# Optimization experiments

Hardware: AMD Instinct MI355X
Metric: run time of the kernel (lower is better)

Reference implementation:

```python
import jax, jax.numpy as jnp
import numpy as np

N_CONST = 188
P = 16
HIDDEN = 128
DE = 5
DO = 6
N_TARGETS = 5
BATCH = 32


def _edge_indices(n):
    # receiver/sender pairs in the same order as itertools.product, skipping diagonal
    r, s = np.meshgrid(np.arange(n), np.arange(n), indexing='ij')
    mask = r != s
    return jnp.asarray(r[mask]), jnp.asarray(s[mask])  # each [n*(n-1)]


def _linear_params(key, fan_in, fan_out):
    kw, kb = jax.random.split(key)
    w = jax.random.normal(kw, (fan_in, fan_out), jnp.float32) / np.sqrt(fan_in)
    b = jax.random.normal(kb, (fan_out,), jnp.float32) * 0.01
    return w, b


def setup_inputs() -> dict:
    key = jax.random.key(0)
    ks = jax.random.split(key, 10)
    inp = {"x": jax.random.normal(ks[0], (BATCH, N_CONST, P), jnp.float32)}
    h2 = HIDDEN // 2
    dims = [
        ("fr1", 2 * P, HIDDEN), ("fr2", HIDDEN, h2), ("fr3", h2, DE),
        ("fo1", P + DE, HIDDEN), ("fo2", HIDDEN, h2), ("fo3", h2, DO),
        ("fc1", DO * N_CONST, HIDDEN), ("fc2", HIDDEN, h2), ("fc3", h2, N_TARGETS),
    ]
    for i, (name, fi, fo) in enumerate(dims):
        w, b = _linear_params(ks[i + 1], fi, fo)
        inp[name + "_w"] = w
        inp[name + "_b"] = b
    return inp


def reference(x, fr1_w, fr1_b, fr2_w, fr2_b, fr3_w, fr3_b,
              fo1_w, fo1_b, fo2_w, fo2_b, fo3_w, fo3_b,
              fc1_w, fc1_b, fc2_w, fc2_b, fc3_w, fc3_b):
    B, n, p = x.shape
    recv, send = _edge_indices(n)  # [Nr]
    # gather receiver/sender node features (replaces one-hot matmuls with Rr, Rs)
    e_in = jnp.concatenate([x[:, recv], x[:, send]], axis=-1)  # [B, Nr, 2P]
    h = jax.nn.relu(e_in @ fr1_w + fr1_b)
    h = jax.nn.relu(h @ fr2_w + fr2_b)
    E = jax.nn.relu(h @ fr3_w + fr3_b)  # [B, Nr, De]
    # scatter-add edge effects back to receiver nodes (replaces E @ Rr^T)
    Ebar = jnp.zeros((B, n, E.shape[-1]), x.dtype).at[:, recv].add(E)  # [B, N, De]
    c = jnp.concatenate([x, Ebar], axis=-1)  # [B, N, P+De]
    h = jax.nn.relu(c @ fo1_w + fo1_b)
    h = jax.nn.relu(h @ fo2_w + fo2_b)
    O = jax.nn.relu(h @ fo3_w + fo3_b)  # [B, N, Do]
    h = jax.nn.relu(O.reshape(B, -1) @ fc1_w + fc1_b)
    h = jax.nn.relu(h @ fc2_w + fc2_b)
    return h @ fc3_w + fc3_b  # [B, n_targets]
```

## Files before the change

kernel.cpp:

```cpp
#include <hip/hip_runtime.h>

#define BB   32
#define NN   188
#define PP   16
#define HID  128
#define HH2  64
#define DE   5
#define DO   6
#define NT   5
#define ROWS_O (BB*NN)
#define RT   32
#define KO   (PP+DE)

typedef __attribute__((ext_vector_type(8))) short short8;
typedef __attribute__((ext_vector_type(4))) float float4_;

__device__ __forceinline__ short f2bf(float v) {
    union { float f; unsigned u; } a; a.f = v;
    unsigned r = a.u + 0x7fff + ((a.u >> 16) & 1);
    return (short)(r >> 16);
}
__device__ __forceinline__ unsigned r2u(float v) {
    v = v > 0.f ? v : 0.f;
    return __float_as_uint(v) + 0x8000u;
}
__device__ __forceinline__ unsigned pack_hi16(unsigned hi, unsigned lo) {
    return __builtin_amdgcn_perm(hi, lo, 0x07060302);
}

#define XB_OFF    0
#define XB_ELTS   (BB*NN*24)
#define W1T_OFF   (XB_OFF + XB_ELTS)
#define W1T_ELTS  (HID*40)
#define W2S_OFF   (W1T_OFF + W1T_ELTS)
#define W2S_ELTS  (16*64*8)
#define W3S_OFF   (W2S_OFF + W2S_ELTS)
#define W3S_ELTS  (2*64*8)
#define SHORT_TOTAL (W3S_OFF + W3S_ELTS)
#define WFRAG_UINT4 ((W2S_ELTS + W3S_ELTS) * 2 / 16)

__device__ __forceinline__ int pinv(int pk) {
    return ((pk >> 5) * 2 + (pk & 1)) * 16 + ((pk & 31) >> 1);
}

__global__ void prep_kernel(const float* __restrict__ x,
                            const float* __restrict__ w1,
                            const float* __restrict__ w2,
                            const float* __restrict__ w3,
                            short* __restrict__ ws)
{
    const int i = blockIdx.x * blockDim.x + threadIdx.x;
    const int stride = gridDim.x * blockDim.x;
    for (int idx = i; idx < BB*NN*PP; idx += stride) {
        int row = idx >> 4, k = idx & 15;
        ws[XB_OFF + row*24 + k] = f2bf(x[idx]);
    }
    for (int idx = i; idx < 32*HID; idx += stride) {
        int k = idx >> 7, n = idx & 127;
        ws[W1T_OFF + n*40 + k] = f2bf(w1[idx]);
    }
    for (int idx = i; idx < W2S_ELTS; idx += stride) {
        int f = idx >> 9;
        int l = (idx >> 3) & 63;
        int e = idx & 7;
        int t = f >> 2, s = f & 3;
        int q = l >> 4, n16 = l & 15;
        int pk = s*32 + q*8 + e;
        int k = pinv(pk);
        int n = t*16 + n16;
        ws[W2S_OFF + idx] = f2bf(w2[k*HH2 + n]);
    }
    for (int idx = i; idx < W3S_ELTS; idx += stride) {
        int s = idx >> 9;
        int l = (idx >> 3) & 63;
        int e = idx & 7;
        int q = l >> 4, n16 = l & 15;
        int pk = s*32 + q*8 + e;
        int k = pinv(pk);
        ws[W3S_OFF + idx] = (n16 < DE) ? f2bf(w3[k*DE + n16]) : (short)0;
    }
}

__global__ __launch_bounds__(256)
void edge_mfma_kernel(const short* __restrict__ ws_s,
                      const float* __restrict__ b1,
                      const float* __restrict__ b2,
                      const float* __restrict__ b3,
                      float* __restrict__ ebar)
{
    const short* xb  = ws_s + XB_OFF;
    const short* w1t = ws_s + W1T_OFF;

    __shared__ __align__(16) unsigned wsmem[4608];
    __shared__ __align__(16) unsigned h1d[4][16*68];
    __shared__ __align__(16) unsigned h2d[4][16*36];
    __shared__ float red[4][8];

    const int bi   = blockIdx.x;
    const int b    = bi / NN;
    const int recv = bi - b*NN;
    const int tid  = threadIdx.x;
    const int wave = tid >> 6;
    const int lane = tid & 63;
    const int n16  = lane & 15;
    const int q    = lane >> 4;

    {
        const uint4* src = (const uint4*)(ws_s + W2S_OFF);
        uint4* dst = (uint4*)wsmem;
        #pragma unroll
        for (int i = 0; i < 5; ++i) {
            int idx = tid + i*256;
            if (idx < WFRAG_UINT4) dst[idx] = src[idx];
        }
    }

    short8 B1[8];
    #pragma unroll
    for (int t = 0; t < 8; ++t)
        B1[t] = *(const short8*)(w1t + (t*16 + n16)*40 + q*8);

    float bias1[8];
    #pragma unroll
    for (int t = 0; t < 8; ++t) bias1[t] = b1[t*16 + n16];
    float bias2[4];
    #pragma unroll
    for (int t = 0; t < 4; ++t) bias2[t] = b2[t*16 + n16];
    const float bias3 = (n16 < DE) ? b3[n16] : 0.f;

    __syncthreads();

    const short* w2l = (const short*)wsmem;
    const short* w3l = (const short*)(wsmem + 4096);
    short8 B3[2];
    #pragma unroll
    for (int s = 0; s < 2; ++s)
        B3[s] = *(const short8*)(w3l + s*512 + lane*8);

    const short* xrow = xb + b*(NN*24);
    unsigned* h1w = &h1d[wave][0];
    unsigned* h2w = &h2d[wave][0];
    const short* h1r = (const short*)h1w;
    const short* h2r = (const short*)h2w;

    float acc[4] = {0.f, 0.f, 0.f, 0.f};

    #pragma unroll
    for (int ti = 0; ti < 3; ++ti) {
        const int rowbase = (wave*3 + ti) * 16;
        const int r = rowbase + n16;
        int send = r + (r >= recv ? 1 : 0);
        if (send > NN-1) send = NN-1;
        const int node = (q < 2) ? recv : send;
        const int koff = (q & 1) * 8;
        short8 A1 = *(const short8*)(xrow + node*24 + koff);

        #pragma unroll
        for (int m = 0; m < 4; ++m) {
            float4_ Ca = (float4_){bias1[2*m],   bias1[2*m],   bias1[2*m],   bias1[2*m]};
            float4_ Cb = (float4_){bias1[2*m+1], bias1[2*m+1], bias1[2*m+1], bias1[2*m+1]};
            Ca = __builtin_amdgcn_mfma_f32_16x16x32_bf16(A1, B1[2*m],   Ca, 0, 0, 0);
            Cb = __builtin_amdgcn_mfma_f32_16x16x32_bf16(A1, B1[2*m+1], Cb, 0, 0, 0);
            #pragma unroll
            for (int rg = 0; rg < 4; ++rg)
                h1w[(q*4+rg)*68 + m*16 + n16] = pack_hi16(r2u(Cb[rg]), r2u(Ca[rg]));
        }

        short8 A2[4];
        #pragma unroll
        for (int s = 0; s < 4; ++s)
            A2[s] = *(const short8*)(h1r + n16*136 + s*32 + q*8);
        #pragma unroll
        for (int m = 0; m < 2; ++m) {
            float4_ Ca = (float4_){bias2[2*m],   bias2[2*m],   bias2[2*m],   bias2[2*m]};
            float4_ Cb = (float4_){bias2[2*m+1], bias2[2*m+1], bias2[2*m+1], bias2[2*m+1]};
            #pragma unroll
            for (int s = 0; s < 4; ++s) {
                short8 Ba = *(const short8*)(w2l + ((2*m)*4+s)*512 + lane*8);
                short8 Bb = *(const short8*)(w2l + ((2*m+1)*4+s)*512 + lane*8);
                Ca = __builtin_amdgcn_mfma_f32_16x16x32_bf16(A2[s], Ba, Ca, 0, 0, 0);
                Cb = __builtin_amdgcn_mfma_f32_16x16x32_bf16(A2[s], Bb, Cb, 0, 0, 0);
            }
            #pragma unroll
            for (int rg = 0; rg < 4; ++rg)
                h2w[(q*4+rg)*36 + m*16 + n16] = pack_hi16(r2u(Cb[rg]), r2u(Ca[rg]));
        }

        float4_ C3 = (float4_){bias3, bias3, bias3, bias3};
        #pragma unroll
        for (int s = 0; s < 2; ++s) {
            short8 A3 = *(const short8*)(h2r + n16*72 + s*32 + q*8);
            C3 = __builtin_amdgcn_mfma_f32_16x16x32_bf16(A3, B3[s], C3, 0, 0, 0);
        }
        #pragma unroll
        for (int rg = 0; rg < 4; ++rg) {
            const int rowid = rowbase + q*4 + rg;
            float e = C3[rg];
            e = e > 0.f ? e : 0.f;
            acc[rg] += (rowid < NN-1) ? e : 0.f;
        }
    }

    float s = (acc[0] + acc[1]) + (acc[2] + acc[3]);
    s += __shfl_xor(s, 16, 64);
    s += __shfl_xor(s, 32, 64);
    if (lane < DE) red[wave][lane] = s;
    __syncthreads();
    if (wave == 0 && lane < DE) {
        float tot = red[0][lane] + red[1][lane] + red[2][lane] + red[3][lane];
        ebar[bi*DE + lane] = tot;
    }
}

__global__ __launch_bounds__(512)
void obj_mlp_kernel(const float* __restrict__ x, const float* __restrict__ ebar,
                    const float* __restrict__ w1, const float* __restrict__ b1,
                    const float* __restrict__ w2, const float* __restrict__ b2,
                    const float* __restrict__ w3, const float* __restrict__ b3,
                    float* __restrict__ o_out)
{
    __shared__ float sW[HID*HH2];
    __shared__ float sB1[HID];
    __shared__ float sB2[HH2];
    __shared__ float sCin[RT*KO];
    __shared__ float sH1[RT*HID];
    __shared__ float sH2t[HH2*(RT+1)];
    const int tid = threadIdx.x;
    const int rbase = blockIdx.x * RT;

    for (int i = tid; i < KO*HID; i += 512) sW[i] = w1[i];
    if (tid < HID) sB1[tid] = b1[tid];
    else if (tid < HID+HH2) sB2[tid-HID] = b2[tid-HID];
    for (int i = tid; i < RT*KO; i += 512) {
        int r = i / KO, k = i - r*KO;
        int gr = rbase + r;
        int b = gr / NN;
        int node = gr - b*NN;
        sCin[i] = (k < PP) ? x[(b*NN+node)*PP + k]
                           : ebar[(b*NN+node)*DE + (k-PP)];
    }
    __syncthreads();

    {
        const int j = tid & (HID-1);
        const int g = tid >> 7;
        float w[KO];
        #pragma unroll
        for (int k = 0; k < KO; ++k) w[k] = sW[k*HID + j];
        const float bj = sB1[j];
        #pragma unroll
        for (int rr = 0; rr < 8; ++rr) {
            const int r = g*8 + rr;
            const float* e = &sCin[r*KO];
            float a0=0.f,a1=0.f,a2=0.f;
            #pragma unroll
            for (int k = 0; k < KO; k += 3) {
                a0 += w[k+0]*e[k+0];
                a1 += w[k+1]*e[k+1];
                a2 += w[k+2]*e[k+2];
            }
            float v = a0+a1+a2+bj;
            sH1[r*HID + j] = v > 0.f ? v : 0.f;
        }
    }
    __syncthreads();
    for (int i = tid; i < HID*HH2; i += 512) sW[i] = w2[i];
    __syncthreads();

    {
        const int j = tid & (HH2-1);
        const int g = tid >> 6;
        float acc[4];
        #pragma unroll
        for (int rr = 0; rr < 4; ++rr) acc[rr] = sB2[j];
        #pragma unroll
        for (int kc = 0; kc < HID; kc += 32) {
            float w[32];
            #pragma unroll
            for (int kk = 0; kk < 32; ++kk) w[kk] = sW[(kc+kk)*HH2 + j];
            #pragma unroll
            for (int rr = 0; rr < 4; ++rr) {
                const float* h = &sH1[(g*4+rr)*HID + kc];
                float a0=0.f,a1=0.f,a2=0.f,a3=0.f;
                #pragma unroll
                for (int kk = 0; kk < 32; kk += 4) {
                    a0 += w[kk+0]*h[kk+0];
                    a1 += w[kk+1]*h[kk+1];
                    a2 += w[kk+2]*h[kk+2];
                    a3 += w[kk+3]*h[kk+3];
                }
                acc[rr] += (a0+a1)+(a2+a3);
            }
        }
        #pragma unroll
        for (int rr = 0; rr < 4; ++rr) {
            float v = acc[rr];
            sH2t[j*(RT+1) + (g*4+rr)] = v > 0.f ? v : 0.f;
        }
    }
    __syncthreads();

    if (tid < RT*DO) {
        const int r = tid & (RT-1);
        const int c = tid >> 5;
        float a0=0.f,a1=0.f,a2=0.f,a3=0.f;
        #pragma unroll
        for (int k = 0; k < HH2; k += 4) {
            a0 += sH2t[(k+0)*(RT+1)+r]*w3[(k+0)*DO+c];
            a1 += sH2t[(k+1)*(RT+1)+r]*w3[(k+1)*DO+c];
            a2 += sH2t[(k+2)*(RT+1)+r]*w3[(k+2)*DO+c];
            a3 += sH2t[(k+3)*(RT+1)+r]*w3[(k+3)*DO+c];
        }
        float v = (a0+a1)+(a2+a3) + b3[c];
        v = v > 0.f ? v : 0.f;
        int gr = rbase + r;
        int b = gr / NN;
        int node = gr - b*NN;
        o_out[b*(NN*DO) + node*DO + c] = v;
    }
}

__global__ __launch_bounds__(256)
void fc_kernel(const float* __restrict__ o_in,
               const float* __restrict__ w1, const float* __restrict__ b1,
               const float* __restrict__ w2, const float* __restrict__ b2,
               const float* __restrict__ w3, const float* __restrict__ b3,
               float* __restrict__ out)
{
    __shared__ __align__(16) float s_in[NN*DO];
    __shared__ float s_p[256];
    __shared__ float s_h1[HID];
    __shared__ float s_h2[HH2];
    const int b = blockIdx.x, tid = threadIdx.x;

    for (int i = tid; i < NN*DO; i += 256) s_in[i] = o_in[b*(NN*DO) + i];
    __syncthreads();

    {
        const int j = tid & (HID-1);
        const int h = tid >> 7;
        const float4* s4 = (const float4*)&s_in[h*564];
        const float* wbase = w1 + (size_t)(h*564)*HID + j;
        float a0=0.f,a1=0.f,a2=0.f,a3=0.f;
        #pragma unroll 4
        for (int i = 0; i < 141; ++i) {
            float4 v = s4[i];
            const float* wp = wbase + (size_t)i*4*HID;
            a0 += v.x * wp[0];
            a1 += v.y * wp[HID];
            a2 += v.z * wp[2*HID];
            a3 += v.w * wp[3*HID];
        }
        s_p[tid] = (a0+a1)+(a2+a3);
    }
    __syncthreads();
    if (tid < HID) {
        float v = s_p[tid] + s_p[tid+HID] + b1[tid];
        s_h1[tid] = v > 0.f ? v : 0.f;
    }
    __syncthreads();

    {
        const int j = tid & (HH2-1);
        const int q = tid >> 6;
        float acc = 0.f;
        #pragma unroll
        for (int kk = 0; kk < 32; ++kk) {
            int k = q*32 + kk;
            acc += s_h1[k] * w2[k*HH2 + j];
        }
        s_p[tid] = acc;
    }
    __syncthreads();
    if (tid < HH2) {
        float v = s_p[tid] + s_p[tid+64] + s_p[tid+128] + s_p[tid+192] + b2[tid];
        s_h2[tid] = v > 0.f ? v : 0.f;
    }
    __syncthreads();

    if (tid < NT) {
        float acc = b3[tid];
        #pragma unroll
        for (int k = 0; k < HH2; ++k)
            acc += s_h2[k] * w3[k*NT + tid];
        out[b*NT + tid] = acc;
    }
}

extern "C" void kernel_launch(void* const* d_in, const int* in_sizes, int n_in,
                              void* d_out, int out_size, void* d_ws, size_t ws_size,
                              hipStream_t stream) {
    (void)in_sizes; (void)n_in; (void)out_size; (void)ws_size;
    const float* x     = (const float*)d_in[0];
    const float* fr1_w = (const float*)d_in[1];
    const float* fr1_b = (const float*)d_in[2];
    const float* fr2_w = (const float*)d_in[3];
    const float* fr2_b = (const float*)d_in[4];
    const float* fr3_w = (const float*)d_in[5];
    const float* fr3_b = (const float*)d_in[6];
    const float* fo1_w = (const float*)d_in[7];
    const float* fo1_b = (const float*)d_in[8];
    const float* fo2_w = (const float*)d_in[9];
    const float* fo2_b = (const float*)d_in[10];
    const float* fo3_w = (const float*)d_in[11];
    const float* fo3_b = (const float*)d_in[12];
    const float* fc1_w = (const float*)d_in[13];
    const float* fc1_b = (const float*)d_in[14];
    const float* fc2_w = (const float*)d_in[15];
    const float* fc2_b = (const float*)d_in[16];
    const float* fc3_w = (const float*)d_in[17];
    const float* fc3_b = (const float*)d_in[18];

    short* ws_s = (short*)d_ws;
    size_t fbase = ((size_t)SHORT_TOTAL*2 + 15) & ~(size_t)15;
    float* ebar = (float*)((char*)d_ws + fbase);
    float* o_ws = ebar + BB*NN*DE;

    prep_kernel<<<128, 256, 0, stream>>>(x, fr1_w, fr2_w, fr3_w, ws_s);
    edge_mfma_kernel<<<BB*NN, 256, 0, stream>>>(ws_s, fr1_b, fr2_b, fr3_b, ebar);
    obj_mlp_kernel<<<ROWS_O/RT, 512, 0, stream>>>(
        x, ebar, fo1_w, fo1_b, fo2_w, fo2_b, fo3_w, fo3_b, o_ws);
    fc_kernel<<<BB, 256, 0, stream>>>(
        o_ws, fc1_w, fc1_b, fc2_w, fc2_b, fc3_w, fc3_b, (float*)d_out);
}
```

Before: 184.6 us.

## Stream edge MLP layer-1 output through layer 2 in K-halves to shrink LDS

The edge kernel now computes the first hidden layer in two 64-wide halves, stages each half in a smaller LDS buffer, and accumulates it into the layer-2 outputs before starting the next half. Layer-2 results are likewise staged 32 columns at a time into a half-size buffer, each slice feeding one layer-3 MFMA. Halving the per-wave LDS scratch is meant to raise occupancy and interleave MFMA work with LDS traffic. In exchange it keeps four layer-2 accumulators live, which adds register pressure, and reuses the scratch buffers within a wave with no explicit barrier between writes and reads.

New measurement: 210.6 us. 1.14x slower.

```diff
diff --git a/kernel.cpp b/kernel.cpp
--- a/kernel.cpp
+++ b/kernel.cpp
@@ -92,9 +92,9 @@
     const short* w1t = ws_s + W1T_OFF;
 
     __shared__ __align__(16) unsigned wsmem[4608];
-    __shared__ __align__(16) unsigned h1d[4][16*68];
-    __shared__ __align__(16) unsigned h2d[4][16*36];
-    __shared__ float red[4][8];
+    __shared__ __align__(16) unsigned h1d[4][16*34];
+    __shared__ __align__(16) unsigned h2d[4][16*18];
+    __shared__ float red[4][DE];
 
     const int bi   = blockIdx.x;
     const int b    = bi / NN;
@@ -140,8 +140,8 @@
     const short* xrow = xb + b*(NN*24);
     unsigned* h1w = &h1d[wave][0];
     unsigned* h2w = &h2d[wave][0];
-    const short* h1r = (const short*)h1w;
-    const short* h2r = (const short*)h2w;
+    const short* h1r = (const short*)&h1d[wave][0];
+    const short* h2r = (const short*)&h2d[wave][0];
 
     float acc[4] = {0.f, 0.f, 0.f, 0.f};
 
@@ -155,42 +155,43 @@
         const int koff = (q & 1) * 8;
         short8 A1 = *(const short8*)(xrow + node*24 + koff);
 
-        #pragma unroll
-        for (int m = 0; m < 4; ++m) {
-            float4_ Ca = (float4_){bias1[2*m],   bias1[2*m],   bias1[2*m],   bias1[2*m]};
-            float4_ Cb = (float4_){bias1[2*m+1], bias1[2*m+1], bias1[2*m+1], bias1[2*m+1]};
-            Ca = __builtin_amdgcn_mfma_f32_16x16x32_bf16(A1, B1[2*m],   Ca, 0, 0, 0);
-            Cb = __builtin_amdgcn_mfma_f32_16x16x32_bf16(A1, B1[2*m+1], Cb, 0, 0, 0);
+        float4_ C2[4];
+        #pragma unroll
+        for (int t = 0; t < 4; ++t)
+            C2[t] = (float4_){bias2[t], bias2[t], bias2[t], bias2[t]};
+
+        #pragma unroll
+        for (int half = 0; half < 2; ++half) {
+            #pragma unroll
+            for (int mm = 0; mm < 2; ++mm) {
+                const int t0 = half*4 + 2*mm;
+                float4_ Ca = (float4_){bias1[t0],   bias1[t0],   bias1[t0],   bias1[t0]};
+                float4_ Cb = (float4_){bias1[t0+1], bias1[t0+1], bias1[t0+1], bias1[t0+1]};
+                Ca = __builtin_amdgcn_mfma_f32_16x16x32_bf16(A1, B1[t0],   Ca, 0, 0, 0);
+                Cb = __builtin_amdgcn_mfma_f32_16x16x32_bf16(A1, B1[t0+1], Cb, 0, 0, 0);
+                #pragma unroll
+                for (int rg = 0; rg < 4; ++rg)
+                    h1w[(q*4+rg)*34 + mm*16 + n16] = pack_hi16(r2u(Cb[rg]), r2u(Ca[rg]));
+            }
+            short8 A2a = *(const short8*)(h1r + n16*68 +      q*8);
+            short8 A2b = *(const short8*)(h1r + n16*68 + 32 + q*8);
+            #pragma unroll
+            for (int t = 0; t < 4; ++t) {
+                short8 Ba = *(const short8*)(w2l + (t*4 + half*2 + 0)*512 + lane*8);
+                short8 Bb = *(const short8*)(w2l + (t*4 + half*2 + 1)*512 + lane*8);
+                C2[t] = __builtin_amdgcn_mfma_f32_16x16x32_bf16(A2a, Ba, C2[t], 0, 0, 0);
+                C2[t] = __builtin_amdgcn_mfma_f32_16x16x32_bf16(A2b, Bb, C2[t], 0, 0, 0);
+            }
+        }
+
+        float4_ C3 = (float4_){bias3, bias3, bias3, bias3};
+        #pragma unroll
+        for (int m = 0; m < 2; ++m) {
             #pragma unroll
             for (int rg = 0; rg < 4; ++rg)
-                h1w[(q*4+rg)*68 + m*16 + n16] = pack_hi16(r2u(Cb[rg]), r2u(Ca[rg]));
-        }
-
-        short8 A2[4];
-        #pragma unroll
-        for (int s = 0; s < 4; ++s)
-            A2[s] = *(const short8*)(h1r + n16*136 + s*32 + q*8);
-        #pragma unroll
-        for (int m = 0; m < 2; ++m) {
-            float4_ Ca = (float4_){bias2[2*m],   bias2[2*m],   bias2[2*m],   bias2[2*m]};
-            float4_ Cb = (float4_){bias2[2*m+1], bias2[2*m+1], bias2[2*m+1], bias2[2*m+1]};
-            #pragma unroll
-            for (int s = 0; s < 4; ++s) {
-                short8 Ba = *(const short8*)(w2l + ((2*m)*4+s)*512 + lane*8);
-                short8 Bb = *(const short8*)(w2l + ((2*m+1)*4+s)*512 + lane*8);
-                Ca = __builtin_amdgcn_mfma_f32_16x16x32_bf16(A2[s], Ba, Ca, 0, 0, 0);
-                Cb = __builtin_amdgcn_mfma_f32_16x16x32_bf16(A2[s], Bb, Cb, 0, 0, 0);
-            }
-            #pragma unroll
-            for (int rg = 0; rg < 4; ++rg)
-                h2w[(q*4+rg)*36 + m*16 + n16] = pack_hi16(r2u(Cb[rg]), r2u(Ca[rg]));
-        }
-
-        float4_ C3 = (float4_){bias3, bias3, bias3, bias3};
-        #pragma unroll
-        for (int s = 0; s < 2; ++s) {
-            short8 A3 = *(const short8*)(h2r + n16*72 + s*32 + q*8);
-            C3 = __builtin_amdgcn_mfma_f32_16x16x32_bf16(A3, B3[s], C3, 0, 0, 0);
+                h2w[(q*4+rg)*18 + n16] = pack_hi16(r2u(C2[2*m+1][rg]), r2u(C2[2*m][rg]));
+            short8 A3 = *(const short8*)(h2r + n16*36 + q*8);
+            C3 = __builtin_amdgcn_mfma_f32_16x16x32_bf16(A3, B3[m], C3, 0, 0, 0);
         }
         #pragma unroll
         for (int rg = 0; rg < 4; ++rg) {
```

## Chain edge MLP layers in registers via transposed MFMA, dropping LDS staging

Applied to the files above, without the earlier changes.

Reformulates the edge MLP so each layer is computed transposed (weights as A operand, activations as B). The MFMA accumulator layout of one layer then feeds the next layer's B fragment directly after bf16 packing. This removes the per-wave LDS round trips for the hidden activations h1 and h2, and the W2/W3 prep is re-permuted to match. Biases now come in as vectors, and the final reduction shuffles across the n16 lanes instead of the q groups. The main risk is correctness of the new K permutation and extra register pressure from the live C2 accumulators.

New measurement: 173.4 us. -6.0%, faster.

```diff
diff --git a/kernel.cpp b/kernel.cpp
--- a/kernel.cpp
+++ b/kernel.cpp
@@ -14,6 +14,7 @@
 
 typedef __attribute__((ext_vector_type(8))) short short8;
 typedef __attribute__((ext_vector_type(4))) float float4_;
+typedef __attribute__((ext_vector_type(4))) unsigned uint4_;
 
 __device__ __forceinline__ short f2bf(float v) {
     union { float f; unsigned u; } a; a.f = v;
@@ -37,10 +38,9 @@
 #define W3S_OFF   (W2S_OFF + W2S_ELTS)
 #define W3S_ELTS  (2*64*8)
 #define SHORT_TOTAL (W3S_OFF + W3S_ELTS)
-#define WFRAG_UINT4 ((W2S_ELTS + W3S_ELTS) * 2 / 16)
-
-__device__ __forceinline__ int pinv(int pk) {
-    return ((pk >> 5) * 2 + (pk & 1)) * 16 + ((pk & 31) >> 1);
+
+__device__ __forceinline__ int kmap(int q, int e) {
+    return (e < 4) ? (q*4 + e) : (16 + q*4 + (e - 4));
 }
 
 __global__ void prep_kernel(const float* __restrict__ x,
@@ -63,20 +63,18 @@
         int f = idx >> 9;
         int l = (idx >> 3) & 63;
         int e = idx & 7;
-        int t = f >> 2, s = f & 3;
+        int tt = f >> 2, s = f & 3;
         int q = l >> 4, n16 = l & 15;
-        int pk = s*32 + q*8 + e;
-        int k = pinv(pk);
-        int n = t*16 + n16;
+        int k = 32*s + kmap(q, e);
+        int n = tt*16 + n16;
         ws[W2S_OFF + idx] = f2bf(w2[k*HH2 + n]);
     }
     for (int idx = i; idx < W3S_ELTS; idx += stride) {
-        int s = idx >> 9;
+        int s2 = idx >> 9;
         int l = (idx >> 3) & 63;
         int e = idx & 7;
         int q = l >> 4, n16 = l & 15;
-        int pk = s*32 + q*8 + e;
-        int k = pinv(pk);
+        int k = 32*s2 + kmap(q, e);
         ws[W3S_OFF + idx] = (n16 < DE) ? f2bf(w3[k*DE + n16]) : (short)0;
     }
 }
@@ -90,11 +88,11 @@
 {
     const short* xb  = ws_s + XB_OFF;
     const short* w1t = ws_s + W1T_OFF;
-
-    __shared__ __align__(16) unsigned wsmem[4608];
-    __shared__ __align__(16) unsigned h1d[4][16*68];
-    __shared__ __align__(16) unsigned h2d[4][16*36];
-    __shared__ float red[4][8];
+    const short* w3g = ws_s + W3S_OFF;
+
+    __shared__ __align__(16) unsigned wsmem[4096];
+    __shared__ __align__(16) float sB1[HID];
+    __shared__ float red[4][16];
 
     const int bi   = blockIdx.x;
     const int b    = bi / NN;
@@ -109,102 +107,98 @@
         const uint4* src = (const uint4*)(ws_s + W2S_OFF);
         uint4* dst = (uint4*)wsmem;
         #pragma unroll
-        for (int i = 0; i < 5; ++i) {
-            int idx = tid + i*256;
-            if (idx < WFRAG_UINT4) dst[idx] = src[idx];
-        }
-    }
-
-    short8 B1[8];
+        for (int i = 0; i < 4; ++i) dst[tid + i*256] = src[tid + i*256];
+    }
+    if (tid < HID) sB1[tid] = b1[tid];
+
+    short8 W1f[8];
     #pragma unroll
     for (int t = 0; t < 8; ++t)
-        B1[t] = *(const short8*)(w1t + (t*16 + n16)*40 + q*8);
-
-    float bias1[8];
-    #pragma unroll
-    for (int t = 0; t < 8; ++t) bias1[t] = b1[t*16 + n16];
-    float bias2[4];
-    #pragma unroll
-    for (int t = 0; t < 4; ++t) bias2[t] = b2[t*16 + n16];
-    const float bias3 = (n16 < DE) ? b3[n16] : 0.f;
+        W1f[t] = *(const short8*)(w1t + (t*16 + n16)*40 + q*8);
+    short8 W3f[2];
+    #pragma unroll
+    for (int s = 0; s < 2; ++s)
+        W3f[s] = *(const short8*)(w3g + s*512 + lane*8);
+    float4_ bias2v[4];
+    #pragma unroll
+    for (int tt = 0; tt < 4; ++tt)
+        bias2v[tt] = *(const float4_*)(b2 + tt*16 + q*4);
+    float4_ bias3r;
+    #pragma unroll
+    for (int rg = 0; rg < 4; ++rg) {
+        int o = q*4 + rg;
+        bias3r[rg] = (o < DE) ? b3[o] : 0.f;
+    }
 
     __syncthreads();
 
     const short* w2l = (const short*)wsmem;
-    const short* w3l = (const short*)(wsmem + 4096);
-    short8 B3[2];
-    #pragma unroll
-    for (int s = 0; s < 2; ++s)
-        B3[s] = *(const short8*)(w3l + s*512 + lane*8);
-
     const short* xrow = xb + b*(NN*24);
-    unsigned* h1w = &h1d[wave][0];
-    unsigned* h2w = &h2d[wave][0];
-    const short* h1r = (const short*)h1w;
-    const short* h2r = (const short*)h2w;
 
     float acc[4] = {0.f, 0.f, 0.f, 0.f};
 
     #pragma unroll
     for (int ti = 0; ti < 3; ++ti) {
         const int rowbase = (wave*3 + ti) * 16;
-        const int r = rowbase + n16;
-        int send = r + (r >= recv ? 1 : 0);
+        const int e = rowbase + n16;
+        int send = e + (e >= recv ? 1 : 0);
         if (send > NN-1) send = NN-1;
         const int node = (q < 2) ? recv : send;
-        const int koff = (q & 1) * 8;
-        short8 A1 = *(const short8*)(xrow + node*24 + koff);
-
-        #pragma unroll
-        for (int m = 0; m < 4; ++m) {
-            float4_ Ca = (float4_){bias1[2*m],   bias1[2*m],   bias1[2*m],   bias1[2*m]};
-            float4_ Cb = (float4_){bias1[2*m+1], bias1[2*m+1], bias1[2*m+1], bias1[2*m+1]};
-            Ca = __builtin_amdgcn_mfma_f32_16x16x32_bf16(A1, B1[2*m],   Ca, 0, 0, 0);
-            Cb = __builtin_amdgcn_mfma_f32_16x16x32_bf16(A1, B1[2*m+1], Cb, 0, 0, 0);
+        short8 E1 = *(const short8*)(xrow + node*24 + (q & 1)*8);
+
+        float4_ C2[4];
+        #pragma unroll
+        for (int tt = 0; tt < 4; ++tt) C2[tt] = bias2v[tt];
+
+        #pragma unroll
+        for (int s = 0; s < 4; ++s) {
+            float4_ cb0 = *(const float4_*)(sB1 + (2*s)*16   + q*4);
+            float4_ cb1 = *(const float4_*)(sB1 + (2*s+1)*16 + q*4);
+            float4_ Ca = __builtin_amdgcn_mfma_f32_16x16x32_bf16(W1f[2*s],   E1, cb0, 0, 0, 0);
+            float4_ Cb = __builtin_amdgcn_mfma_f32_16x16x32_bf16(W1f[2*s+1], E1, cb1, 0, 0, 0);
+            uint4_ dv = (uint4_){ pack_hi16(r2u(Ca[1]), r2u(Ca[0])),
+                                  pack_hi16(r2u(Ca[3]), r2u(Ca[2])),
+                                  pack_hi16(r2u(Cb[1]), r2u(Cb[0])),
+                                  pack_hi16(r2u(Cb[3]), r2u(Cb[2])) };
+            short8 Bf = __builtin_bit_cast(short8, dv);
             #pragma unroll
-            for (int rg = 0; rg < 4; ++rg)
-                h1w[(q*4+rg)*68 + m*16 + n16] = pack_hi16(r2u(Cb[rg]), r2u(Ca[rg]));
-        }
-
-        short8 A2[4];
-        #pragma unroll
-        for (int s = 0; s < 4; ++s)
-            A2[s] = *(const short8*)(h1r + n16*136 + s*32 + q*8);
-        #pragma unroll
-        for (int m = 0; m < 2; ++m) {
-            float4_ Ca = (float4_){bias2[2*m],   bias2[2*m],   bias2[2*m],   bias2[2*m]};
-            float4_ Cb = (float4_){bias2[2*m+1], bias2[2*m+1], bias2[2*m+1], bias2[2*m+1]};
-            #pragma unroll
-            for (int s = 0; s < 4; ++s) {
-                short8 Ba = *(const short8*)(w2l + ((2*m)*4+s)*512 + lane*8);
-                short8 Bb = *(const short8*)(w2l + ((2*m+1)*4+s)*512 + lane*8);
-                Ca = __builtin_amdgcn_mfma_f32_16x16x32_bf16(A2[s], Ba, Ca, 0, 0, 0);
-                Cb = __builtin_amdgcn_mfma_f32_16x16x32_bf16(A2[s], Bb, Cb, 0, 0, 0);
+            for (int tt = 0; tt < 4; ++tt) {
+                short8 A2 = *(const short8*)(w2l + (tt*4 + s)*512 + lane*8);
+                C2[tt] = __builtin_amdgcn_mfma_f32_16x16x32_bf16(A2, Bf, C2[tt], 0, 0, 0);
             }
-            #pragma unroll
-            for (int rg = 0; rg < 4; ++rg)
-                h2w[(q*4+rg)*36 + m*16 + n16] = pack_hi16(r2u(Cb[rg]), r2u(Ca[rg]));
-        }
-
-        float4_ C3 = (float4_){bias3, bias3, bias3, bias3};
-        #pragma unroll
-        for (int s = 0; s < 2; ++s) {
-            short8 A3 = *(const short8*)(h2r + n16*72 + s*32 + q*8);
-            C3 = __builtin_amdgcn_mfma_f32_16x16x32_bf16(A3, B3[s], C3, 0, 0, 0);
-        }
+        }
+
+        float4_ C3 = bias3r;
+        #pragma unroll
+        for (int s2 = 0; s2 < 2; ++s2) {
+            float4_ Cc = C2[2*s2], Cd = C2[2*s2+1];
+            uint4_ dv = (uint4_){ pack_hi16(r2u(Cc[1]), r2u(Cc[0])),
+                                  pack_hi16(r2u(Cc[3]), r2u(Cc[2])),
+                                  pack_hi16(r2u(Cd[1]), r2u(Cd[0])),
+                                  pack_hi16(r2u(Cd[3]), r2u(Cd[2])) };
+            short8 B3f = __builtin_bit_cast(short8, dv);
+            C3 = __builtin_amdgcn_mfma_f32_16x16x32_bf16(W3f[s2], B3f, C3, 0, 0, 0);
+        }
+        const bool ok = (e < NN-1);
         #pragma unroll
         for (int rg = 0; rg < 4; ++rg) {
-            const int rowid = rowbase + q*4 + rg;
-            float e = C3[rg];
-            e = e > 0.f ? e : 0.f;
-            acc[rg] += (rowid < NN-1) ? e : 0.f;
-        }
-    }
-
-    float s = (acc[0] + acc[1]) + (acc[2] + acc[3]);
-    s += __shfl_xor(s, 16, 64);
-    s += __shfl_xor(s, 32, 64);
-    if (lane < DE) red[wave][lane] = s;
+            float v = C3[rg];
+            v = v > 0.f ? v : 0.f;
+            acc[rg] += ok ? v : 0.f;
+        }
+    }
+
+    #pragma unroll
+    for (int rg = 0; rg < 4; ++rg) {
+        acc[rg] += __shfl_xor(acc[rg], 1);
+        acc[rg] += __shfl_xor(acc[rg], 2);
+        acc[rg] += __shfl_xor(acc[rg], 4);
+        acc[rg] += __shfl_xor(acc[rg], 8);
+    }
+    if (n16 == 0) {
+        #pragma unroll
+        for (int rg = 0; rg < 4; ++rg) red[wave][q*4 + rg] = acc[rg];
+    }
     __syncthreads();
     if (wave == 0 && lane < DE) {
         float tot = red[0][lane] + red[1][lane] + red[2][lane] + red[3][lane];
```
